# Optimization experiments

Hardware: AMD Instinct MI355X
Metric: run time of the kernel (lower is better)

The kernel has to match this reference:

```python
import jax, jax.numpy as jnp
import numpy as np

N, E, D = 100000, 600000, 128
BN_EPS = 1e-5


def setup_inputs() -> dict:
    key = jax.random.key(0)
    ks = jax.random.split(key, 8)
    x = jax.random.normal(ks[0], (N, D), dtype=jnp.float32)
    edge_index = jax.random.randint(ks[1], (2, E), 0, N, dtype=jnp.int64)
    # learned params: GIN eps (train_eps=True, init 0), Linear-BN-Linear MLP
    eps = jnp.zeros((), dtype=jnp.float32)
    s = 1.0 / np.sqrt(D)
    W1 = jax.random.uniform(ks[2], (D, D), jnp.float32, -s, s)
    b1 = jax.random.uniform(ks[3], (D,), jnp.float32, -s, s)
    gamma = jnp.ones((D,), jnp.float32)
    beta = jnp.zeros((D,), jnp.float32)
    W2 = jax.random.uniform(ks[4], (D, D), jnp.float32, -s, s)
    b2 = jax.random.uniform(ks[5], (D,), jnp.float32, -s, s)
    return {"x": x, "edge_index": edge_index, "eps": eps, "W1": W1, "b1": b1,
            "gamma": gamma, "beta": beta, "W2": W2, "b2": b2}


def reference(x, edge_index, eps, W1, b1, gamma, beta, W2, b2):
    src, dst = edge_index[0], edge_index[1]
    n = x.shape[0]
    # GIN aggregation: sum of neighbor features scattered to target nodes
    agg = jax.ops.segment_sum(x[src], dst, num_segments=n)  # [N, D]
    h = (1.0 + eps) * x + agg
    # MLP: Linear -> BatchNorm1d (training-mode batch stats) -> ReLU -> Linear
    h = h @ W1.T + b1
    mean = jnp.mean(h, axis=0)
    var = jnp.mean(jnp.square(h - mean), axis=0)  # biased variance, as BN uses
    h = (h - mean) * jax.lax.rsqrt(var + BN_EPS) * gamma + beta
    h = jax.nn.relu(h)
    h = h @ W2.T + b2
    # outer residual with ReLU
    return x + jax.nn.relu(h)
```

## Files before the change

kernel.cpp:

```cpp
#include <hip/hip_runtime.h>
#include <hip/hip_bf16.h>


typedef __attribute__((ext_vector_type(8))) short short8;
typedef __attribute__((ext_vector_type(4))) float f32x4;

static __device__ __forceinline__ float bf2f(unsigned short u) {
    union { unsigned int i; float f; } z; z.i = ((unsigned int)u) << 16; return z.f;
}
static __device__ __forceinline__ unsigned short f2bf(float f) {
    unsigned int u = __float_as_uint(f);
    unsigned int lsb = (u >> 16) & 1u;
    u += 0x7fffu + lsb;
    return (unsigned short)(u >> 16);
}
static __device__ __forceinline__ void atomAdd(float* p, float v) {
    __hip_atomic_fetch_add(p, v, __ATOMIC_RELAXED, __HIP_MEMORY_SCOPE_AGENT);
}

__global__ __launch_bounds__(256) void k_detect(const unsigned short* __restrict__ gamma,
                                                const int* __restrict__ ei,
                                                int* __restrict__ flags,
                                                float* __restrict__ stats,
                                                int* __restrict__ counts, int N) {
    int idx = blockIdx.x * 256 + threadIdx.x;
    if (idx < N) counts[idx] = 0;
    if (blockIdx.x == 0) {
        int t = threadIdx.x;
        if (t < 256) stats[t] = 0.0f;
        if (t == 0) {
            flags[0] = (gamma[0] == 0x3F80u) ? 0 : 1;
            int odd = ei[1] | ei[3] | ei[5] | ei[7] | ei[9] | ei[11] | ei[13] | ei[15];
            flags[1] = (odd == 0) ? 1 : 0;
        }
    }
}

__global__ __launch_bounds__(256) void k_hist(const int* __restrict__ ei, int* __restrict__ counts,
                                              int E, const int* __restrict__ flags) {
    int e = blockIdx.x * 256 + threadIdx.x;
    if (e >= E) return;
    int dst = flags[1] ? ei[2 * E + 2 * e] : ei[E + e];
    atomicAdd(&counts[dst], 1);
}

__global__ __launch_bounds__(256) void k_scan1(const int* __restrict__ counts, int* __restrict__ partA,
                                               int N) {
    __shared__ int sd[256];
    int t = threadIdx.x, idx = blockIdx.x * 256 + t;
    sd[t] = (idx < N) ? counts[idx] : 0;
    __syncthreads();
    for (int off = 128; off > 0; off >>= 1) {
        if (t < off) sd[t] += sd[t + off];
        __syncthreads();
    }
    if (t == 0) partA[blockIdx.x] = sd[0];
}

__global__ __launch_bounds__(512) void k_scan2(const int* __restrict__ partA, int* __restrict__ partB,
                                               int NB) {
    __shared__ int sd[512];
    int t = threadIdx.x;
    sd[t] = (t < NB) ? partA[t] : 0;
    __syncthreads();
    for (int off = 1; off < 512; off <<= 1) {
        int v = (t >= off) ? sd[t - off] : 0;
        __syncthreads();
        sd[t] += v;
        __syncthreads();
    }
    if (t < NB) partB[t] = sd[t] - partA[t];
}

__global__ __launch_bounds__(256) void k_scan3(int* __restrict__ counts, int* __restrict__ rowptr,
                                               const int* __restrict__ partB, int N) {
    __shared__ int sd[256];
    int t = threadIdx.x, idx = blockIdx.x * 256 + t;
    int c = (idx < N) ? counts[idx] : 0;
    sd[t] = c;
    __syncthreads();
    for (int off = 1; off < 256; off <<= 1) {
        int v = (t >= off) ? sd[t - off] : 0;
        __syncthreads();
        sd[t] += v;
        __syncthreads();
    }
    int offB = partB[blockIdx.x];
    int excl = offB + sd[t] - c;
    if (idx < N) {
        rowptr[idx] = excl;
        counts[idx] = excl;
        if (idx == N - 1) rowptr[N] = excl + c;
    }
}

__global__ __launch_bounds__(256) void k_fill(const int* __restrict__ ei, int* __restrict__ cursor,
                                              int* __restrict__ bucket, int E,
                                              const int* __restrict__ flags) {
    int e = blockIdx.x * 256 + threadIdx.x;
    if (e >= E) return;
    int src, dst;
    if (flags[1]) { src = ei[2 * e]; dst = ei[2 * E + 2 * e]; }
    else          { src = ei[e];     dst = ei[E + e]; }
    int pos = atomicAdd(&cursor[dst], 1);
    bucket[pos] = src;
}

__global__ __launch_bounds__(256) void k_gather(const void* __restrict__ x,
                                                const void* __restrict__ eps,
                                                const int* __restrict__ rowptr,
                                                const int* __restrict__ bucket,
                                                unsigned int* __restrict__ h0, int N,
                                                const int* __restrict__ flags) {
    int wave = threadIdx.x >> 6, lane = threadIdx.x & 63;
    int n = blockIdx.x * 4 + wave;
    if (n >= N) return;
    int mode = flags[0];
    int beg = rowptr[n], end = rowptr[n + 1];
    float ax = 0.f, ay = 0.f;
    if (mode == 0) {
        const unsigned int* xr = (const unsigned int*)x;
        int e = beg;
        for (; e + 4 <= end; e += 4) {
            int s0 = bucket[e], s1 = bucket[e + 1], s2 = bucket[e + 2], s3 = bucket[e + 3];
            unsigned int u0 = xr[(size_t)s0 * 64 + lane];
            unsigned int u1 = xr[(size_t)s1 * 64 + lane];
            unsigned int u2 = xr[(size_t)s2 * 64 + lane];
            unsigned int u3 = xr[(size_t)s3 * 64 + lane];
            ax += (bf2f((unsigned short)(u0 & 0xffffu)) + bf2f((unsigned short)(u1 & 0xffffu)))
                + (bf2f((unsigned short)(u2 & 0xffffu)) + bf2f((unsigned short)(u3 & 0xffffu)));
            ay += (bf2f((unsigned short)(u0 >> 16)) + bf2f((unsigned short)(u1 >> 16)))
                + (bf2f((unsigned short)(u2 >> 16)) + bf2f((unsigned short)(u3 >> 16)));
        }
        if (e + 2 <= end) {
            int s0 = bucket[e], s1 = bucket[e + 1];
            unsigned int u0 = xr[(size_t)s0 * 64 + lane];
            unsigned int u1 = xr[(size_t)s1 * 64 + lane];
            ax += bf2f((unsigned short)(u0 & 0xffffu)) + bf2f((unsigned short)(u1 & 0xffffu));
            ay += bf2f((unsigned short)(u0 >> 16)) + bf2f((unsigned short)(u1 >> 16));
            e += 2;
        }
        if (e < end) {
            unsigned int u = xr[(size_t)bucket[e] * 64 + lane];
            ax += bf2f((unsigned short)(u & 0xffffu));
            ay += bf2f((unsigned short)(u >> 16));
        }
        float s = 1.0f + bf2f(((const unsigned short*)eps)[0]);
        unsigned int u = xr[(size_t)n * 64 + lane];
        ax = fmaf(s, bf2f((unsigned short)(u & 0xffffu)), ax);
        ay = fmaf(s, bf2f((unsigned short)(u >> 16)), ay);
    } else {
        const float2* xr = (const float2*)x;
        int e = beg;
        for (; e + 4 <= end; e += 4) {
            int s0 = bucket[e], s1 = bucket[e + 1], s2 = bucket[e + 2], s3 = bucket[e + 3];
            float2 v0 = xr[(size_t)s0 * 64 + lane];
            float2 v1 = xr[(size_t)s1 * 64 + lane];
            float2 v2 = xr[(size_t)s2 * 64 + lane];
            float2 v3 = xr[(size_t)s3 * 64 + lane];
            ax += (v0.x + v1.x) + (v2.x + v3.x);
            ay += (v0.y + v1.y) + (v2.y + v3.y);
        }
        for (; e < end; ++e) {
            float2 v = xr[(size_t)bucket[e] * 64 + lane];
            ax += v.x; ay += v.y;
        }
        float s = 1.0f + ((const float*)eps)[0];
        float2 v = xr[(size_t)n * 64 + lane];
        ax = fmaf(s, v.x, ax);
        ay = fmaf(s, v.y, ay);
    }
    h0[(size_t)n * 64 + lane] = (unsigned int)f2bf(ax) | ((unsigned int)f2bf(ay) << 16);
}

static __device__ __forceinline__ void stageW(const void* W, unsigned short* Wl,
                                              int tid, int mode) {
    for (int c = tid; c < 2048; c += 256) {
        int li = c & 15, kg = (c >> 4) & 15, t = c >> 8;
        int srcOff = (t * 16 + li) * 128 + kg * 8;
        if (mode == 0) {
            *(short8*)&Wl[c * 8] = *(const short8*)((const unsigned short*)W + srcOff);
        } else {
            const float4* wf = (const float4*)((const float*)W + srcOff);
            float4 f0 = wf[0], f1 = wf[1];
            union { short8 v; unsigned short s[8]; } u;
            u.s[0] = f2bf(f0.x); u.s[1] = f2bf(f0.y); u.s[2] = f2bf(f0.z); u.s[3] = f2bf(f0.w);
            u.s[4] = f2bf(f1.x); u.s[5] = f2bf(f1.y); u.s[6] = f2bf(f1.z); u.s[7] = f2bf(f1.w);
            *(short8*)&Wl[c * 8] = u.v;
        }
    }
}

__global__ __launch_bounds__(256) void k_gemm1(const unsigned short* __restrict__ h0,
                                               const void* __restrict__ W1,
                                               const void* __restrict__ b1,
                                               unsigned short* __restrict__ h1,
                                               float* __restrict__ stats,
                                               int N, const int* __restrict__ flags) {
    __shared__ unsigned short Wl[16384];
    __shared__ float bl[128];
    __shared__ float red_s[4][128], red_s2[4][128];
    int tid = threadIdx.x;
    int mode = flags[0];
    stageW(W1, Wl, tid, mode);
    if (tid < 128)
        bl[tid] = mode ? ((const float*)b1)[tid] : bf2f(((const unsigned short*)b1)[tid]);
    __syncthreads();

    int lane = tid & 63, wave = tid >> 6;
    int li = lane & 15, q = lane >> 4;
    float s_acc[8] = {0.f, 0.f, 0.f, 0.f, 0.f, 0.f, 0.f, 0.f};
    float s2_acc[8] = {0.f, 0.f, 0.f, 0.f, 0.f, 0.f, 0.f, 0.f};

#pragma unroll
    for (int rt = 0; rt < 2; ++rt) {
        int m0 = blockIdx.x * 128 + (wave + rt * 4) * 16;
        int rowA = m0 + li; if (rowA >= N) rowA = N - 1;
        const unsigned short* ap = h0 + (size_t)rowA * 128 + q * 8;

        f32x4 acc[8] = {};
#pragma unroll
        for (int c4 = 0; c4 < 4; ++c4) {
            short8 av = *(const short8*)(ap + c4 * 32);
#pragma unroll
            for (int t = 0; t < 8; ++t) {
                short8 bfrag = *(const short8*)&Wl[(t * 256 + (c4 * 4 + q) * 16 + li) * 8];
                acc[t] = __builtin_amdgcn_mfma_f32_16x16x32_bf16(av, bfrag, acc[t], 0, 0, 0);
            }
        }
#pragma unroll
        for (int t = 0; t < 8; ++t) {
            int col = t * 16 + li;
            float bb = bl[col];
#pragma unroll
            for (int r = 0; r < 4; ++r) {
                int row = m0 + q * 4 + r;
                if (row < N) {
                    float v = acc[t][r] + bb;
                    h1[(size_t)row * 128 + col] = f2bf(v);
                    s_acc[t] += v; s2_acc[t] += v * v;
                }
            }
        }
    }
#pragma unroll
    for (int t = 0; t < 8; ++t) {
        float s = s_acc[t], s2 = s2_acc[t];
        s  += __shfl_xor(s, 16);  s  += __shfl_xor(s, 32);
        s2 += __shfl_xor(s2, 16); s2 += __shfl_xor(s2, 32);
        if (lane < 16) { red_s[wave][t * 16 + li] = s; red_s2[wave][t * 16 + li] = s2; }
    }
    __syncthreads();
    if (tid < 128) {
        atomAdd(&stats[tid], red_s[0][tid] + red_s[1][tid] + red_s[2][tid] + red_s[3][tid]);
    } else {
        int c = tid - 128;
        atomAdd(&stats[tid], red_s2[0][c] + red_s2[1][c] + red_s2[2][c] + red_s2[3][c]);
    }
}

__global__ __launch_bounds__(256) void k_gemm2(const unsigned short* __restrict__ h1,
                                               const void* __restrict__ W2,
                                               const void* __restrict__ b2,
                                               const float* __restrict__ stats,
                                               const void* __restrict__ gamma,
                                               const void* __restrict__ beta,
                                               const void* __restrict__ x,
                                               void* __restrict__ out, int N, float invN,
                                               const int* __restrict__ flags) {
    __shared__ unsigned short Wl[16384];
    __shared__ float bl[128], al[128], cl[128];
    int tid = threadIdx.x;
    int mode = flags[0];
    stageW(W2, Wl, tid, mode);
    if (tid < 128) {
        bl[tid] = mode ? ((const float*)b2)[tid] : bf2f(((const unsigned short*)b2)[tid]);
        float mean = stats[tid] * invN;
        float var = stats[128 + tid] * invN - mean * mean;
        float g  = mode ? ((const float*)gamma)[tid] : bf2f(((const unsigned short*)gamma)[tid]);
        float bt = mode ? ((const float*)beta)[tid]  : bf2f(((const unsigned short*)beta)[tid]);
        float a = g * rsqrtf(var + 1e-5f);
        al[tid] = a;
        cl[tid] = bt - mean * a;
    }
    __syncthreads();

    int lane = tid & 63, wave = tid >> 6;
    int li = lane & 15, q = lane >> 4;

#pragma unroll
    for (int rt = 0; rt < 2; ++rt) {
        int m0 = blockIdx.x * 128 + (wave + rt * 4) * 16;
        int rowA = m0 + li; if (rowA >= N) rowA = N - 1;
        const unsigned short* ap = h1 + (size_t)rowA * 128 + q * 8;

        f32x4 acc[8] = {};
#pragma unroll
        for (int c4 = 0; c4 < 4; ++c4) {
            int k0 = c4 * 32 + q * 8;
            union { short8 v; unsigned short s[8]; } hu;
            hu.v = *(const short8*)(ap + c4 * 32);
            float4 sa = *(const float4*)&al[k0];
            float4 sb = *(const float4*)&al[k0 + 4];
            float4 ca = *(const float4*)&cl[k0];
            float4 cb = *(const float4*)&cl[k0 + 4];
            union { short8 v; unsigned short s[8]; } au;
            au.s[0] = f2bf(fmaxf(fmaf(bf2f(hu.s[0]), sa.x, ca.x), 0.f));
            au.s[1] = f2bf(fmaxf(fmaf(bf2f(hu.s[1]), sa.y, ca.y), 0.f));
            au.s[2] = f2bf(fmaxf(fmaf(bf2f(hu.s[2]), sa.z, ca.z), 0.f));
            au.s[3] = f2bf(fmaxf(fmaf(bf2f(hu.s[3]), sa.w, ca.w), 0.f));
            au.s[4] = f2bf(fmaxf(fmaf(bf2f(hu.s[4]), sb.x, cb.x), 0.f));
            au.s[5] = f2bf(fmaxf(fmaf(bf2f(hu.s[5]), sb.y, cb.y), 0.f));
            au.s[6] = f2bf(fmaxf(fmaf(bf2f(hu.s[6]), sb.z, cb.z), 0.f));
            au.s[7] = f2bf(fmaxf(fmaf(bf2f(hu.s[7]), sb.w, cb.w), 0.f));
#pragma unroll
            for (int t = 0; t < 8; ++t) {
                short8 bfrag = *(const short8*)&Wl[(t * 256 + (c4 * 4 + q) * 16 + li) * 8];
                acc[t] = __builtin_amdgcn_mfma_f32_16x16x32_bf16(au.v, bfrag, acc[t], 0, 0, 0);
            }
        }
#pragma unroll
        for (int t = 0; t < 8; ++t) {
            int col = t * 16 + li;
            float bb = bl[col];
#pragma unroll
            for (int r = 0; r < 4; ++r) {
                int row = m0 + q * 4 + r;
                if (row < N) {
                    size_t idx = (size_t)row * 128 + col;
                    float v = fmaxf(acc[t][r] + bb, 0.f);
                    if (mode == 0) {
                        float xv = bf2f(((const unsigned short*)x)[idx]);
                        ((unsigned short*)out)[idx] = f2bf(xv + v);
                    } else {
                        float xv = ((const float*)x)[idx];
                        ((float*)out)[idx] = xv + v;
                    }
                }
            }
        }
    }
}

extern "C" void kernel_launch(void* const* d_in, const int* in_sizes, int n_in,
                              void* d_out, int out_size, void* d_ws, size_t ws_size,
                              hipStream_t stream) {
    const void* x     = d_in[0];
    const int*  ei    = (const int*)d_in[1];
    const void* eps   = d_in[2];
    const void* W1    = d_in[3];
    const void* b1    = d_in[4];
    const void* gamma = d_in[5];
    const void* beta  = d_in[6];
    const void* W2    = d_in[7];
    const void* b2    = d_in[8];

    int N = in_sizes[0] / 128;
    int E = in_sizes[1] / 2;

    unsigned short* h0 = (unsigned short*)d_ws;
    unsigned short* h1 = h0 + (size_t)N * 128;
    int* counts = (int*)(h1 + (size_t)N * 128);
    int* rowptr = counts + N;
    int* bucket = rowptr + N + 1;
    int* partA  = bucket + E;
    int* partB  = partA + 512;
    float* stats = (float*)(partB + 512);
    int*   flags = (int*)(stats + 256);

    int NB = (N + 255) / 256;
    int EB = (E + 255) / 256;

    k_detect<<<NB, 256, 0, stream>>>((const unsigned short*)gamma, ei, flags, stats, counts, N);
    k_hist<<<EB, 256, 0, stream>>>(ei, counts, E, flags);
    k_scan1<<<NB, 256, 0, stream>>>(counts, partA, N);
    k_scan2<<<1, 512, 0, stream>>>(partA, partB, NB);
    k_scan3<<<NB, 256, 0, stream>>>(counts, rowptr, partB, N);
    k_fill<<<EB, 256, 0, stream>>>(ei, counts, bucket, E, flags);

    k_gather<<<(N + 3) / 4, 256, 0, stream>>>(x, eps, rowptr, bucket,
                                              (unsigned int*)h0, N, flags);

    int mb = (N + 127) / 128;
    k_gemm1<<<mb, 256, 0, stream>>>(h0, W1, b1, h1, stats, N, flags);
    k_gemm2<<<mb, 256, 0, stream>>>(h1, W2, b2, stats, gamma, beta, x, d_out, N,
                                    1.0f / (float)N, flags);
}
```

Baseline: 320.6 us.

## Drop scan2 kernel, batch gather loads by 8, prefetch GEMM A tiles

Three separate changes. First, the single-block scan2 launch is removed: each scan3 block now sums the preceding partial block sums itself. Second, the gather loop now issues eight masked neighbor loads per iteration instead of four plus tails, to keep more memory requests in flight. Third, both GEMM kernels load their A-operand fragments into registers before staging W into LDS, so the global loads overlap with W staging. The trade-offs are redundant partial-sum reads in scan3 (up to about 390 per block), wasted clamped loads in the gather tail, and higher register pressure in the GEMMs.

```diff
diff --git a/kernel.cpp b/kernel.cpp
--- a/kernel.cpp
+++ b/kernel.cpp
@@ -57,25 +57,20 @@
     if (t == 0) partA[blockIdx.x] = sd[0];
 }
 
-__global__ __launch_bounds__(512) void k_scan2(const int* __restrict__ partA, int* __restrict__ partB,
-                                               int NB) {
-    __shared__ int sd[512];
-    int t = threadIdx.x;
-    sd[t] = (t < NB) ? partA[t] : 0;
-    __syncthreads();
-    for (int off = 1; off < 512; off <<= 1) {
-        int v = (t >= off) ? sd[t - off] : 0;
+__global__ __launch_bounds__(256) void k_scan3(int* __restrict__ counts, int* __restrict__ rowptr,
+                                               const int* __restrict__ partA, int N) {
+    __shared__ int sd[256];
+    int t = threadIdx.x, b = blockIdx.x, idx = b * 256 + t;
+    int acc = 0;
+    for (int j = t; j < b; j += 256) acc += partA[j];
+    sd[t] = acc;
+    __syncthreads();
+    for (int off = 128; off > 0; off >>= 1) {
+        if (t < off) sd[t] += sd[t + off];
         __syncthreads();
-        sd[t] += v;
-        __syncthreads();
-    }
-    if (t < NB) partB[t] = sd[t] - partA[t];
-}
-
-__global__ __launch_bounds__(256) void k_scan3(int* __restrict__ counts, int* __restrict__ rowptr,
-                                               const int* __restrict__ partB, int N) {
-    __shared__ int sd[256];
-    int t = threadIdx.x, idx = blockIdx.x * 256 + t;
+    }
+    int offB = sd[0];
+    __syncthreads();
     int c = (idx < N) ? counts[idx] : 0;
     sd[t] = c;
     __syncthreads();
@@ -85,7 +80,6 @@
         sd[t] += v;
         __syncthreads();
     }
-    int offB = partB[blockIdx.x];
     int excl = offB + sd[t] - c;
     if (idx < N) {
         rowptr[idx] = excl;
@@ -120,30 +114,21 @@
     float ax = 0.f, ay = 0.f;
     if (mode == 0) {
         const unsigned int* xr = (const unsigned int*)x;
-        int e = beg;
-        for (; e + 4 <= end; e += 4) {
-            int s0 = bucket[e], s1 = bucket[e + 1], s2 = bucket[e + 2], s3 = bucket[e + 3];
-            unsigned int u0 = xr[(size_t)s0 * 64 + lane];
-            unsigned int u1 = xr[(size_t)s1 * 64 + lane];
-            unsigned int u2 = xr[(size_t)s2 * 64 + lane];
-            unsigned int u3 = xr[(size_t)s3 * 64 + lane];
-            ax += (bf2f((unsigned short)(u0 & 0xffffu)) + bf2f((unsigned short)(u1 & 0xffffu)))
-                + (bf2f((unsigned short)(u2 & 0xffffu)) + bf2f((unsigned short)(u3 & 0xffffu)));
-            ay += (bf2f((unsigned short)(u0 >> 16)) + bf2f((unsigned short)(u1 >> 16)))
-                + (bf2f((unsigned short)(u2 >> 16)) + bf2f((unsigned short)(u3 >> 16)));
-        }
-        if (e + 2 <= end) {
-            int s0 = bucket[e], s1 = bucket[e + 1];
-            unsigned int u0 = xr[(size_t)s0 * 64 + lane];
-            unsigned int u1 = xr[(size_t)s1 * 64 + lane];
-            ax += bf2f((unsigned short)(u0 & 0xffffu)) + bf2f((unsigned short)(u1 & 0xffffu));
-            ay += bf2f((unsigned short)(u0 >> 16)) + bf2f((unsigned short)(u1 >> 16));
-            e += 2;
-        }
-        if (e < end) {
-            unsigned int u = xr[(size_t)bucket[e] * 64 + lane];
-            ax += bf2f((unsigned short)(u & 0xffffu));
-            ay += bf2f((unsigned short)(u >> 16));
+        for (int e = beg; e < end; e += 8) {
+            int idx8[8]; bool mk[8];
+#pragma unroll
+            for (int k = 0; k < 8; ++k) {
+                int ee = e + k;
+                mk[k] = ee < end;
+                idx8[k] = bucket[mk[k] ? ee : end - 1];
+            }
+#pragma unroll
+            for (int k = 0; k < 8; ++k) {
+                unsigned int u = xr[(size_t)idx8[k] * 64 + lane];
+                float fx = bf2f((unsigned short)(u & 0xffffu));
+                float fy = bf2f((unsigned short)(u >> 16));
+                if (mk[k]) { ax += fx; ay += fy; }
+            }
         }
         float s = 1.0f + bf2f(((const unsigned short*)eps)[0]);
         unsigned int u = xr[(size_t)n * 64 + lane];
@@ -151,19 +136,19 @@
         ay = fmaf(s, bf2f((unsigned short)(u >> 16)), ay);
     } else {
         const float2* xr = (const float2*)x;
-        int e = beg;
-        for (; e + 4 <= end; e += 4) {
-            int s0 = bucket[e], s1 = bucket[e + 1], s2 = bucket[e + 2], s3 = bucket[e + 3];
-            float2 v0 = xr[(size_t)s0 * 64 + lane];
-            float2 v1 = xr[(size_t)s1 * 64 + lane];
-            float2 v2 = xr[(size_t)s2 * 64 + lane];
-            float2 v3 = xr[(size_t)s3 * 64 + lane];
-            ax += (v0.x + v1.x) + (v2.x + v3.x);
-            ay += (v0.y + v1.y) + (v2.y + v3.y);
-        }
-        for (; e < end; ++e) {
-            float2 v = xr[(size_t)bucket[e] * 64 + lane];
-            ax += v.x; ay += v.y;
+        for (int e = beg; e < end; e += 8) {
+            int idx8[8]; bool mk[8];
+#pragma unroll
+            for (int k = 0; k < 8; ++k) {
+                int ee = e + k;
+                mk[k] = ee < end;
+                idx8[k] = bucket[mk[k] ? ee : end - 1];
+            }
+#pragma unroll
+            for (int k = 0; k < 8; ++k) {
+                float2 v = xr[(size_t)idx8[k] * 64 + lane];
+                if (mk[k]) { ax += v.x; ay += v.y; }
+            }
         }
         float s = 1.0f + ((const float*)eps)[0];
         float2 v = xr[(size_t)n * 64 + lane];
@@ -202,30 +187,37 @@
     __shared__ float red_s[4][128], red_s2[4][128];
     int tid = threadIdx.x;
     int mode = flags[0];
+    int lane = tid & 63, wave = tid >> 6;
+    int li = lane & 15, q = lane >> 4;
+
+    short8 av[2][4];
+#pragma unroll
+    for (int rt = 0; rt < 2; ++rt) {
+        int rowA = blockIdx.x * 128 + (wave + rt * 4) * 16 + li;
+        if (rowA >= N) rowA = N - 1;
+        const unsigned short* ap = h0 + (size_t)rowA * 128 + q * 8;
+#pragma unroll
+        for (int c4 = 0; c4 < 4; ++c4) av[rt][c4] = *(const short8*)(ap + c4 * 32);
+    }
+
     stageW(W1, Wl, tid, mode);
     if (tid < 128)
         bl[tid] = mode ? ((const float*)b1)[tid] : bf2f(((const unsigned short*)b1)[tid]);
     __syncthreads();
 
-    int lane = tid & 63, wave = tid >> 6;
-    int li = lane & 15, q = lane >> 4;
     float s_acc[8] = {0.f, 0.f, 0.f, 0.f, 0.f, 0.f, 0.f, 0.f};
     float s2_acc[8] = {0.f, 0.f, 0.f, 0.f, 0.f, 0.f, 0.f, 0.f};
 
 #pragma unroll
     for (int rt = 0; rt < 2; ++rt) {
         int m0 = blockIdx.x * 128 + (wave + rt * 4) * 16;
-        int rowA = m0 + li; if (rowA >= N) rowA = N - 1;
-        const unsigned short* ap = h0 + (size_t)rowA * 128 + q * 8;
-
         f32x4 acc[8] = {};
 #pragma unroll
         for (int c4 = 0; c4 < 4; ++c4) {
-            short8 av = *(const short8*)(ap + c4 * 32);
 #pragma unroll
             for (int t = 0; t < 8; ++t) {
                 short8 bfrag = *(const short8*)&Wl[(t * 256 + (c4 * 4 + q) * 16 + li) * 8];
-                acc[t] = __builtin_amdgcn_mfma_f32_16x16x32_bf16(av, bfrag, acc[t], 0, 0, 0);
+                acc[t] = __builtin_amdgcn_mfma_f32_16x16x32_bf16(av[rt][c4], bfrag, acc[t], 0, 0, 0);
             }
         }
 #pragma unroll
@@ -272,6 +264,19 @@
     __shared__ float bl[128], al[128], cl[128];
     int tid = threadIdx.x;
     int mode = flags[0];
+    int lane = tid & 63, wave = tid >> 6;
+    int li = lane & 15, q = lane >> 4;
+
+    short8 hv[2][4];
+#pragma unroll
+    for (int rt = 0; rt < 2; ++rt) {
+        int rowA = blockIdx.x * 128 + (wave + rt * 4) * 16 + li;
+        if (rowA >= N) rowA = N - 1;
+        const unsigned short* ap = h1 + (size_t)rowA * 128 + q * 8;
+#pragma unroll
+        for (int c4 = 0; c4 < 4; ++c4) hv[rt][c4] = *(const short8*)(ap + c4 * 32);
+    }
+
     stageW(W2, Wl, tid, mode);
     if (tid < 128) {
         bl[tid] = mode ? ((const float*)b2)[tid] : bf2f(((const unsigned short*)b2)[tid]);
@@ -285,21 +290,15 @@
     }
     __syncthreads();
 
-    int lane = tid & 63, wave = tid >> 6;
-    int li = lane & 15, q = lane >> 4;
-
 #pragma unroll
     for (int rt = 0; rt < 2; ++rt) {
         int m0 = blockIdx.x * 128 + (wave + rt * 4) * 16;
-        int rowA = m0 + li; if (rowA >= N) rowA = N - 1;
-        const unsigned short* ap = h1 + (size_t)rowA * 128 + q * 8;
-
         f32x4 acc[8] = {};
 #pragma unroll
         for (int c4 = 0; c4 < 4; ++c4) {
             int k0 = c4 * 32 + q * 8;
             union { short8 v; unsigned short s[8]; } hu;
-            hu.v = *(const short8*)(ap + c4 * 32);
+            hu.v = hv[rt][c4];
             float4 sa = *(const float4*)&al[k0];
             float4 sb = *(const float4*)&al[k0 + 4];
             float4 ca = *(const float4*)&cl[k0];
@@ -364,8 +363,7 @@
     int* rowptr = counts + N;
     int* bucket = rowptr + N + 1;
     int* partA  = bucket + E;
-    int* partB  = partA + 512;
-    float* stats = (float*)(partB + 512);
+    float* stats = (float*)(partA + 512);
     int*   flags = (int*)(stats + 256);
 
     int NB = (N + 255) / 256;
@@ -374,8 +372,7 @@
     k_detect<<<NB, 256, 0, stream>>>((const unsigned short*)gamma, ei, flags, stats, counts, N);
     k_hist<<<EB, 256, 0, stream>>>(ei, counts, E, flags);
     k_scan1<<<NB, 256, 0, stream>>>(counts, partA, N);
-    k_scan2<<<1, 512, 0, stream>>>(partA, partB, NB);
-    k_scan3<<<NB, 256, 0, stream>>>(counts, rowptr, partB, N);
+    k_scan3<<<NB, 256, 0, stream>>>(counts, rowptr, partA, N);
     k_fill<<<EB, 256, 0, stream>>>(ei, counts, bucket, E, flags);
 
     k_gather<<<(N + 3) / 4, 256, 0, stream>>>(x, eps, rowptr, bucket,
```

Measured after the change: 335.0 us. 1.05x slower.
